# Optimization experiments

Measured on AMD Instinct MI355X. Metric: run time of the kernel, lower is better.

The kernel has to match this reference:

```python
import jax, jax.numpy as jnp
import numpy as np

B, H, W, DIM = 2, 64, 64, 128
NH = 4
HD = DIM // NH
KS = 7
DIL = 2
SCALE = HD ** -0.5


def _natten_idx(L, k, dil):
    """Per-position neighborhood start + rpb start (NATTEN semantics), as gather index tables."""
    ns = k // 2
    starts = np.empty(L, np.int32)
    pbs = np.empty(L, np.int32)
    for i in range(L):
        if dil <= 1:
            s = max(i - ns, 0) + (i + ns >= L) * (L - i - ns - 1)
            p = ns + (i < ns) * (ns - i) + (i + ns >= L) * (L - i - 1 - ns)
        else:
            if i - ns * dil < 0:
                s = i % dil
                p = k - 1 - (i // dil)
            elif i + ns * dil >= L:
                imodd = i % dil
                a = (L // dil) * dil
                b = L - a
                if imodd < b:
                    s = L - b + imodd - 2 * ns * dil
                else:
                    s = a + imodd - k * dil
                p = (L - i - 1) // dil
            else:
                s = i - ns * dil
                p = ns
        starts[i] = s
        pbs[i] = p
    key_idx = starts[:, None] + dil * np.arange(k, dtype=np.int32)  # [L, k] key positions
    pb_idx = pbs[:, None] + np.arange(k, dtype=np.int32)            # [L, k] rpb positions
    return key_idx, pb_idx


def setup_inputs() -> dict:
    key = jax.random.key(0)
    ks = jax.random.split(key, 12)
    shp = (B, H, W, DIM)
    q = jax.random.normal(ks[0], shp, jnp.float32)
    k = jax.random.normal(ks[1], shp, jnp.float32)
    v = jax.random.normal(ks[2], shp, jnp.float32)
    def lin(kk):
        return jax.random.normal(kk, (DIM, DIM), jnp.float32) * (DIM ** -0.5)
    Wq, Wk, Wv, Wo = lin(ks[3]), lin(ks[4]), lin(ks[5]), lin(ks[6])
    bq = jnp.zeros((DIM,), jnp.float32)
    bk = jnp.zeros((DIM,), jnp.float32)
    bv = jnp.zeros((DIM,), jnp.float32)
    bo = jnp.zeros((DIM,), jnp.float32)
    rpb = jax.random.normal(ks[7], (NH, 2 * KS - 1, 2 * KS - 1), jnp.float32) * 0.02
    return {"q": q, "k": k, "v": v, "Wq": Wq, "bq": bq, "Wk": Wk, "bk": bk,
            "Wv": Wv, "bv": bv, "rpb": rpb, "Wo": Wo, "bo": bo}


def _forward(q, k, v, Wq, bq, Wk, bk, Wv, bv, rpb, Wo, bo):
    Bc, Hc, Wc, C = q.shape
    ii, pi = _natten_idx(Hc, KS, DIL)   # [H, K]
    jj, pj = _natten_idx(Wc, KS, DIL)   # [W, K]

    def heads(x, Wm, bm):
        # [B,H,W,C] -> [B,NH,H,W,HD]
        return (x @ Wm + bm).reshape(Bc, Hc, Wc, NH, HD).transpose(0, 3, 1, 2, 4)

    qh = heads(q, Wq, bq) * SCALE
    kh = heads(k, Wk, bk)
    vh = heads(v, Wv, bv)

    # Gather KxK dilated neighborhoods: [B,NH,H,K,W,K,HD]
    knbr = kh[:, :, ii][:, :, :, :, jj]
    vnbr = vh[:, :, ii][:, :, :, :, jj]

    # attention logits per pixel over its KxK neighborhood: [B,NH,H,W,K,K]
    attn = jnp.einsum('bnhwd,bnhkwld->bnhwkl', qh, knbr)
    # relative position bias lookup: [NH,H,K,W,K] -> [NH,H,W,K,K]
    bias = rpb[:, pi][:, :, :, pj].transpose(0, 1, 3, 2, 4)
    attn = attn + bias[None]

    attn = jax.nn.softmax(attn.reshape(Bc, NH, Hc, Wc, KS * KS), axis=-1)
    attn = attn.reshape(Bc, NH, Hc, Wc, KS, KS)

    out = jnp.einsum('bnhwkl,bnhkwld->bnhwd', attn, vnbr)
    out = out.transpose(0, 2, 3, 1, 4).reshape(Bc, Hc, Wc, C)
    return out @ Wo + bo


def reference(q, k, v, Wq, bq, Wk, bk, Wv, bv, rpb, Wo, bo):
    return _forward(q, k, v, Wq, bq, Wk, bk, Wv, bv, rpb, Wo, bo)
```

## Files before the change

kernel.cpp:

```cpp
#include <hip/hip_runtime.h>
#include <hip/hip_bf16.h>
#include <math.h>

#define BB 2
#define HH 64
#define WW 64
#define DIMC 128
#define NH 4
#define HD 32
#define KS 7
#define DIL 2
#define NPIX (BB * HH * WW)
#define SCALE 0.17677669529663687f

typedef short bf16x8 __attribute__((ext_vector_type(8)));
typedef float f32x4  __attribute__((ext_vector_type(4)));

__device__ __forceinline__ short bf16r(float f) {
    union { float f; unsigned u; } x; x.f = f;
    unsigned r = x.u + 0x7FFF + ((x.u >> 16) & 1);
    return (short)(r >> 16);
}
__device__ __forceinline__ float uasf(unsigned u) {
    union { unsigned u; float f; } x; x.u = u; return x.f;
}

__global__ __launch_bounds__(256) void prep_w(
    const float* __restrict__ Wq, const float* __restrict__ Wk,
    const float* __restrict__ Wv, const float* __restrict__ Wo,
    short* __restrict__ Wt)
{
    const int z  = blockIdx.x >> 2;
    const int ks = blockIdx.x & 3;
    const float* W = (z == 0) ? Wq : (z == 1) ? Wk : (z == 2) ? Wv : Wo;

    __shared__ short T[32][136];
    const int t = threadIdx.x;
    const float4* Wg = (const float4*)(W + ks * 32 * 128);

    float4 xv[4];
#pragma unroll
    for (int u = 0; u < 4; ++u) xv[u] = Wg[u * 256 + t];
#pragma unroll
    for (int u = 0; u < 4; ++u) {
        const int e = u * 256 + t;
        const int r = e >> 5;
        const int c = (e & 31) * 4;
        short4 s4;
        s4.x = bf16r(xv[u].x); s4.y = bf16r(xv[u].y);
        s4.z = bf16r(xv[u].z); s4.w = bf16r(xv[u].w);
        *(short4*)&T[r][c] = s4;
    }
    __syncthreads();

    const int c = t >> 1;
    const int h = (t & 1) * 16;
    bf16x8 lo, hi;
#pragma unroll
    for (int i = 0; i < 8; ++i) { lo[i] = T[h + i][c]; hi[i] = T[h + 8 + i][c]; }
    short* outp = Wt + z * 16384 + c * 128 + ks * 32 + h;
    *(bf16x8*)(outp)     = lo;
    *(bf16x8*)(outp + 8) = hi;
}

__global__ __launch_bounds__(256) void qkv_mfma(
    const float* __restrict__ q, const float* __restrict__ k,
    const float* __restrict__ v, const short* __restrict__ Wt,
    const float* __restrict__ bq, const float* __restrict__ bk,
    const float* __restrict__ bv,
    float* __restrict__ qh, short* __restrict__ khb, short* __restrict__ vhb)
{
    const int z = blockIdx.y;
    const float* X    = (z == 0) ? q  : (z == 1) ? k  : v;
    const float* bias = (z == 0) ? bq : (z == 1) ? bk : bv;
    const short* Wz   = Wt + z * 16384;

    const int t    = threadIdx.x;
    const int wv   = t >> 6;
    const int lane = t & 63;
    const int lr   = lane & 15;
    const int lg   = lane >> 4;
    const int row0 = blockIdx.x * 32 + (wv & 1) * 16;
    const int col0 = (wv >> 1) * 64;

    bf16x8 bfr[16];
#pragma unroll
    for (int nt = 0; nt < 4; ++nt) {
        const short* wrow = Wz + (col0 + nt * 16 + lr) * 128 + lg * 8;
#pragma unroll
        for (int kk = 0; kk < 4; ++kk)
            bfr[nt * 4 + kk] = *(const bf16x8*)(wrow + kk * 32);
    }

    const float* xrow = X + (size_t)(row0 + lr) * 128 + lg * 8;
    bf16x8 a[4];
#pragma unroll
    for (int kk = 0; kk < 4; ++kk) {
        const float4 x0 = *(const float4*)(xrow + kk * 32);
        const float4 x1 = *(const float4*)(xrow + kk * 32 + 4);
        bf16x8 av;
        av[0] = bf16r(x0.x); av[1] = bf16r(x0.y);
        av[2] = bf16r(x0.z); av[3] = bf16r(x0.w);
        av[4] = bf16r(x1.x); av[5] = bf16r(x1.y);
        av[6] = bf16r(x1.z); av[7] = bf16r(x1.w);
        a[kk] = av;
    }

#pragma unroll
    for (int nt = 0; nt < 4; ++nt) {
        const int col = col0 + nt * 16 + lr;
        f32x4 acc = {0.f, 0.f, 0.f, 0.f};
#pragma unroll
        for (int kk = 0; kk < 4; ++kk)
            acc = __builtin_amdgcn_mfma_f32_16x16x32_bf16(a[kk], bfr[nt * 4 + kk], acc, 0, 0, 0);
        const float bc = bias[col];
        if (z == 0) {
#pragma unroll
            for (int jj = 0; jj < 4; ++jj)
                qh[(size_t)(row0 + lg * 4 + jj) * 128 + col] = (acc[jj] + bc) * SCALE;
        } else {
            short* Yb = (z == 1) ? khb : vhb;
#pragma unroll
            for (int jj = 0; jj < 4; ++jj)
                Yb[(size_t)(row0 + lg * 4 + jj) * 128 + col] = bf16r(acc[jj] + bc);
        }
    }
}

__device__ __forceinline__ void natten_idx(int i, int& s, int& p)
{
    if (i < 6) {
        s = i & 1;
        p = 6 - (i >> 1);
    } else if (i >= 58) {
        s = 50 + (i & 1);
        p = (63 - i) >> 1;
    } else {
        s = i - 6;
        p = 3;
    }
}

__global__ __launch_bounds__(256) void natten_out(
    const float* __restrict__ qh, const short* __restrict__ khb,
    const short* __restrict__ vhb, const float* __restrict__ rpb,
    const short* __restrict__ Wt, const float* __restrict__ bo,
    float* __restrict__ out)
{
    __shared__ short attS[16][136];

    const int blk  = blockIdx.x;
    const int work = (blk & 7) * 64 + (blk >> 3);
    const int t    = threadIdx.x;

    {
        const int lane4 = t & 3;
        const int n  = (t >> 2) & 3;
        const int p  = t >> 4;
        const int g  = work * 16 + p;
        const int j  = g & 63;
        const int i  = (g >> 6) & 63;
        const int b  = g >> 12;

        int si, pi0, sj, pj0;
        natten_idx(i, si, pi0);
        natten_idx(j, sj, pj0);

        const int coff = n * 32 + lane4 * 8;
        const size_t pixb = (size_t)(b * 4096 + i * 64 + j);
        const float4 q0 = *(const float4*)(qh + pixb * 128 + coff);
        const float4 q1 = *(const float4*)(qh + pixb * 128 + coff + 4);

        const float* rp = rpb + n * 169;

        float m = -1e30f, l = 0.0f;
        float o[8] = {0.f, 0.f, 0.f, 0.f, 0.f, 0.f, 0.f, 0.f};

#pragma unroll
        for (int ki = 0; ki < 7; ++ki) {
            const int iy = si + 2 * ki;
            const size_t rowbase = ((size_t)(b * 4096 + iy * 64)) * 128 + coff;
            const float* rrow = rp + (pi0 + ki) * 13 + pj0;

            float d[7];
#pragma unroll
            for (int kj = 0; kj < 7; ++kj) {
                const int ix = sj + 2 * kj;
                const uint4 kv = *(const uint4*)(khb + rowbase + (size_t)ix * 128);
                float dd =      q0.x * uasf(kv.x << 16);
                dd = fmaf(q0.y, uasf(kv.x & 0xFFFF0000u), dd);
                dd = fmaf(q0.z, uasf(kv.y << 16), dd);
                dd = fmaf(q0.w, uasf(kv.y & 0xFFFF0000u), dd);
                dd = fmaf(q1.x, uasf(kv.z << 16), dd);
                dd = fmaf(q1.y, uasf(kv.z & 0xFFFF0000u), dd);
                dd = fmaf(q1.z, uasf(kv.w << 16), dd);
                dd = fmaf(q1.w, uasf(kv.w & 0xFFFF0000u), dd);
                d[kj] = dd;
            }
#pragma unroll
            for (int kj = 0; kj < 7; ++kj) d[kj] += __shfl_xor(d[kj], 1);
#pragma unroll
            for (int kj = 0; kj < 7; ++kj) d[kj] += __shfl_xor(d[kj], 2);
#pragma unroll
            for (int kj = 0; kj < 7; ++kj) d[kj] += rrow[kj];

            const float g01 = fmaxf(d[0], d[1]);
            const float g23 = fmaxf(d[2], d[3]);
            const float g45 = fmaxf(d[4], d[5]);
            const float gm  = fmaxf(fmaxf(g01, g23), fmaxf(g45, d[6]));
            const float mn  = fmaxf(m, gm);
            const float corr = __expf(m - mn);
            m = mn;
            l *= corr;
#pragma unroll
            for (int e = 0; e < 8; ++e) o[e] *= corr;

#pragma unroll
            for (int kj = 0; kj < 7; ++kj) {
                const float pe = __expf(d[kj] - m);
                d[kj] = pe;
                l += pe;
            }

#pragma unroll
            for (int kj = 0; kj < 7; ++kj) {
                const int ix = sj + 2 * kj;
                const uint4 vv = *(const uint4*)(vhb + rowbase + (size_t)ix * 128);
                const float pe = d[kj];
                o[0] = fmaf(pe, uasf(vv.x << 16),          o[0]);
                o[1] = fmaf(pe, uasf(vv.x & 0xFFFF0000u),  o[1]);
                o[2] = fmaf(pe, uasf(vv.y << 16),          o[2]);
                o[3] = fmaf(pe, uasf(vv.y & 0xFFFF0000u),  o[3]);
                o[4] = fmaf(pe, uasf(vv.z << 16),          o[4]);
                o[5] = fmaf(pe, uasf(vv.z & 0xFFFF0000u),  o[5]);
                o[6] = fmaf(pe, uasf(vv.w << 16),          o[6]);
                o[7] = fmaf(pe, uasf(vv.w & 0xFFFF0000u),  o[7]);
            }
        }

        const float inv = 1.0f / l;
        bf16x8 ow;
#pragma unroll
        for (int e = 0; e < 8; ++e) ow[e] = bf16r(o[e] * inv);
        *(bf16x8*)&attS[p][coff] = ow;
    }

    __syncthreads();

    {
        const int wv   = t >> 6;
        const int lane = t & 63;
        const int lr   = lane & 15;
        const int lg   = lane >> 4;
        const int col0 = wv * 32;
        const short* Wz = Wt + 3 * 16384;

        bf16x8 bfr[8];
#pragma unroll
        for (int nt = 0; nt < 2; ++nt) {
            const short* wrow = Wz + (col0 + nt * 16 + lr) * 128 + lg * 8;
#pragma unroll
            for (int kk = 0; kk < 4; ++kk)
                bfr[nt * 4 + kk] = *(const bf16x8*)(wrow + kk * 32);
        }
        bf16x8 a[4];
#pragma unroll
        for (int kk = 0; kk < 4; ++kk)
            a[kk] = *(const bf16x8*)&attS[lr][kk * 32 + lg * 8];

#pragma unroll
        for (int nt = 0; nt < 2; ++nt) {
            const int col = col0 + nt * 16 + lr;
            f32x4 acc = {0.f, 0.f, 0.f, 0.f};
#pragma unroll
            for (int kk = 0; kk < 4; ++kk)
                acc = __builtin_amdgcn_mfma_f32_16x16x32_bf16(a[kk], bfr[nt * 4 + kk], acc, 0, 0, 0);
            const float bc = bo[col];
#pragma unroll
            for (int jj = 0; jj < 4; ++jj)
                out[(size_t)(work * 16 + lg * 4 + jj) * 128 + col] = acc[jj] + bc;
        }
    }
}

extern "C" void kernel_launch(void* const* d_in, const int* in_sizes, int n_in,
                              void* d_out, int out_size, void* d_ws, size_t ws_size,
                              hipStream_t stream)
{
    const float* q   = (const float*)d_in[0];
    const float* k   = (const float*)d_in[1];
    const float* v   = (const float*)d_in[2];
    const float* Wq  = (const float*)d_in[3];
    const float* bq  = (const float*)d_in[4];
    const float* Wk  = (const float*)d_in[5];
    const float* bk  = (const float*)d_in[6];
    const float* Wv  = (const float*)d_in[7];
    const float* bv  = (const float*)d_in[8];
    const float* rpb = (const float*)d_in[9];
    const float* Wo  = (const float*)d_in[10];
    const float* bo  = (const float*)d_in[11];

    float* ws   = (float*)d_ws;
    float* qh   = ws;
    short* khb  = (short*)(ws + (size_t)NPIX * 128);
    short* vhb  = khb + (size_t)NPIX * 128;
    short* Wt   = vhb + (size_t)NPIX * 128;
    float* out  = (float*)d_out;

    hipLaunchKernelGGL(prep_w, dim3(16), dim3(256), 0, stream, Wq, Wk, Wv, Wo, Wt);

    hipLaunchKernelGGL(qkv_mfma, dim3(256, 3), dim3(256), 0, stream,
                       q, k, v, Wt, bq, bk, bv, qh, khb, vhb);

    hipLaunchKernelGGL(natten_out, dim3(512), dim3(256), 0, stream,
                       qh, khb, vhb, rpb, Wt, bo, out);
}
```

Measured before the change: 35.20 us.

## Compute neighborhood attention with MFMA over a shared-memory key/value window

Replaces the per-pixel scalar FMA neighborhood attention with a block-level scheme: for each head, a 7x28 window of keys is staged into LDS, QK^T for 16 pixels is computed densely with bf16 MFMA, softmax is applied with masking into a sparse P matrix, and P·V is done with MFMA against a transposed V tile. The aim is to swap many redundant global loads and scalar FMAs for shared reuse and matrix instructions. In exchange it computes extra unused scores, rounds Q and P to bf16, adds several barriers per head and leaves many threads idle during softmax and PV.

```diff
diff --git a/kernel.cpp b/kernel.cpp
--- a/kernel.cpp
+++ b/kernel.cpp
@@ -21,9 +21,6 @@
     unsigned r = x.u + 0x7FFF + ((x.u >> 16) & 1);
     return (short)(r >> 16);
 }
-__device__ __forceinline__ float uasf(unsigned u) {
-    union { unsigned u; float f; } x; x.u = u; return x.f;
-}
 
 __global__ __launch_bounds__(256) void prep_w(
     const float* __restrict__ Wq, const float* __restrict__ Wk,
@@ -147,111 +144,159 @@
     const short* __restrict__ Wt, const float* __restrict__ bo,
     float* __restrict__ out)
 {
-    __shared__ short attS[16][136];
+    __shared__ __align__(16) short KT[208 * 40];
+    __shared__ __align__(16) float S[16 * 208];
+    __shared__ __align__(16) short P[16 * 232];
+    __shared__ __align__(16) short Vt[32 * 232];
+    __shared__ __align__(16) short attS[16][136];
 
     const int blk  = blockIdx.x;
     const int work = (blk & 7) * 64 + (blk >> 3);
     const int t    = threadIdx.x;
 
+    const int j0 = (work & 3) * 16;
+    const int i_ = (work >> 2) & 63;
+    const int b_ = work >> 8;
+
+    int si, pi0, sj0v, pj0v;
+    natten_idx(i_, si, pi0);
+    natten_idx(j0, sj0v, pj0v);
+    const int colbase = sj0v;
+
+    const int wv   = t >> 6;
+    const int lane = t & 63;
+    const int lr   = lane & 15;
+    const int lg   = lane >> 4;
+
+    const size_t gbase = (size_t)(b_ * 4096) * 128;
+
+#pragma unroll 1
+    for (int n = 0; n < 4; ++n) {
+        for (int u = t; u < 784; u += 256) {
+            const int key = u >> 2;
+            const int ch4 = (u & 3) * 8;
+            const int ki  = key / 28;
+            const int c   = key - ki * 28;
+            int col = colbase + c; col = (col > 63) ? 63 : col;
+            const int iy = si + 2 * ki;
+            const uint4 kv = *(const uint4*)(khb + gbase +
+                                 (size_t)(iy * 64 + col) * 128 + n * 32 + ch4);
+            *(uint4*)&KT[key * 40 + ch4] = kv;
+        }
+        __syncthreads();
+
+        {
+            const float* qp = qh + (size_t)(b_ * 4096 + i_ * 64 + j0 + lr) * 128
+                              + n * 32 + lg * 8;
+            const float4 x0 = *(const float4*)(qp);
+            const float4 x1 = *(const float4*)(qp + 4);
+            bf16x8 aq;
+            aq[0] = bf16r(x0.x); aq[1] = bf16r(x0.y);
+            aq[2] = bf16r(x0.z); aq[3] = bf16r(x0.w);
+            aq[4] = bf16r(x1.x); aq[5] = bf16r(x1.y);
+            aq[6] = bf16r(x1.z); aq[7] = bf16r(x1.w);
+
+            for (int nb = wv; nb < 13; nb += 4) {
+                const bf16x8 bk = *(const bf16x8*)&KT[(nb * 16 + lr) * 40 + lg * 8];
+                f32x4 sa = {0.f, 0.f, 0.f, 0.f};
+                sa = __builtin_amdgcn_mfma_f32_16x16x32_bf16(aq, bk, sa, 0, 0, 0);
+#pragma unroll
+                for (int jj = 0; jj < 4; ++jj)
+                    S[(lg * 4 + jj) * 208 + nb * 16 + lr] = sa[jj];
+            }
+            unsigned* Pz = (unsigned*)P;
+            for (int u = t; u < 1856; u += 256) Pz[u] = 0u;
+        }
+        __syncthreads();
+
+        if (t < 64) {
+            const int px = t >> 2, q = t & 3;
+            const int j = j0 + px;
+            int sjp, pj0p;
+            natten_idx(j, sjp, pj0p);
+            const int cj0 = sjp - colbase;
+
+            float d[14];
+            float mx = -1e30f;
+#pragma unroll
+            for (int rr = 0; rr < 2; ++rr) {
+                const int ki  = q + rr * 4;
+                const bool ok = (ki < 7);
+                const int kis = ok ? ki : 3;
+                const float* rp = rpb + n * 169 + (pi0 + kis) * 13 + pj0p;
+#pragma unroll
+                for (int kj = 0; kj < 7; ++kj) {
+                    const float s = ok ? (S[px * 208 + kis * 28 + cj0 + 2 * kj] + rp[kj])
+                                       : -1e30f;
+                    d[rr * 7 + kj] = s;
+                    mx = fmaxf(mx, s);
+                }
+            }
+            mx = fmaxf(mx, __shfl_xor(mx, 1));
+            mx = fmaxf(mx, __shfl_xor(mx, 2));
+            float l = 0.f;
+#pragma unroll
+            for (int ii = 0; ii < 14; ++ii) {
+                const float pe = __expf(d[ii] - mx);
+                d[ii] = pe;
+                l += pe;
+            }
+            l += __shfl_xor(l, 1);
+            l += __shfl_xor(l, 2);
+            const float inv = 1.0f / l;
+#pragma unroll
+            for (int rr = 0; rr < 2; ++rr) {
+                const int ki  = q + rr * 4;
+                if (ki < 7) {
+#pragma unroll
+                    for (int kj = 0; kj < 7; ++kj)
+                        P[px * 232 + ki * 28 + cj0 + 2 * kj] = bf16r(d[rr * 7 + kj] * inv);
+                }
+            }
+        } else {
+            for (int u = t - 64; u < 896; u += 192) {
+                const int key = u >> 2;
+                const int ch4 = (u & 3) * 8;
+                if (key < 196) {
+                    const int ki = key / 28;
+                    const int c  = key - ki * 28;
+                    int col = colbase + c; col = (col > 63) ? 63 : col;
+                    const int iy = si + 2 * ki;
+                    const uint4 vv = *(const uint4*)(vhb + gbase +
+                                       (size_t)(iy * 64 + col) * 128 + n * 32 + ch4);
+                    Vt[(ch4 + 0) * 232 + key] = (short)(vv.x & 0xFFFFu);
+                    Vt[(ch4 + 1) * 232 + key] = (short)(vv.x >> 16);
+                    Vt[(ch4 + 2) * 232 + key] = (short)(vv.y & 0xFFFFu);
+                    Vt[(ch4 + 3) * 232 + key] = (short)(vv.y >> 16);
+                    Vt[(ch4 + 4) * 232 + key] = (short)(vv.z & 0xFFFFu);
+                    Vt[(ch4 + 5) * 232 + key] = (short)(vv.z >> 16);
+                    Vt[(ch4 + 6) * 232 + key] = (short)(vv.w & 0xFFFFu);
+                    Vt[(ch4 + 7) * 232 + key] = (short)(vv.w >> 16);
+                } else {
+#pragma unroll
+                    for (int e = 0; e < 8; ++e)
+                        Vt[(ch4 + e) * 232 + key] = 0;
+                }
+            }
+        }
+        __syncthreads();
+
+        if (wv < 2) {
+            f32x4 oa = {0.f, 0.f, 0.f, 0.f};
+#pragma unroll
+            for (int kk = 0; kk < 7; ++kk) {
+                const bf16x8 pa = *(const bf16x8*)&P[lr * 232 + kk * 32 + lg * 8];
+                const bf16x8 vb = *(const bf16x8*)&Vt[(wv * 16 + lr) * 232 + kk * 32 + lg * 8];
+                oa = __builtin_amdgcn_mfma_f32_16x16x32_bf16(pa, vb, oa, 0, 0, 0);
+            }
+#pragma unroll
+            for (int jj = 0; jj < 4; ++jj)
+                attS[lg * 4 + jj][n * 32 + wv * 16 + lr] = bf16r(oa[jj]);
+        }
+        __syncthreads();
+    }
+
     {
-        const int lane4 = t & 3;
-        const int n  = (t >> 2) & 3;
-        const int p  = t >> 4;
-        const int g  = work * 16 + p;
-        const int j  = g & 63;
-        const int i  = (g >> 6) & 63;
-        const int b  = g >> 12;
-
-        int si, pi0, sj, pj0;
-        natten_idx(i, si, pi0);
-        natten_idx(j, sj, pj0);
-
-        const int coff = n * 32 + lane4 * 8;
-        const size_t pixb = (size_t)(b * 4096 + i * 64 + j);
-        const float4 q0 = *(const float4*)(qh + pixb * 128 + coff);
-        const float4 q1 = *(const float4*)(qh + pixb * 128 + coff + 4);
-
-        const float* rp = rpb + n * 169;
-
-        float m = -1e30f, l = 0.0f;
-        float o[8] = {0.f, 0.f, 0.f, 0.f, 0.f, 0.f, 0.f, 0.f};
-
-#pragma unroll
-        for (int ki = 0; ki < 7; ++ki) {
-            const int iy = si + 2 * ki;
-            const size_t rowbase = ((size_t)(b * 4096 + iy * 64)) * 128 + coff;
-            const float* rrow = rp + (pi0 + ki) * 13 + pj0;
-
-            float d[7];
-#pragma unroll
-            for (int kj = 0; kj < 7; ++kj) {
-                const int ix = sj + 2 * kj;
-                const uint4 kv = *(const uint4*)(khb + rowbase + (size_t)ix * 128);
-                float dd =      q0.x * uasf(kv.x << 16);
-                dd = fmaf(q0.y, uasf(kv.x & 0xFFFF0000u), dd);
-                dd = fmaf(q0.z, uasf(kv.y << 16), dd);
-                dd = fmaf(q0.w, uasf(kv.y & 0xFFFF0000u), dd);
-                dd = fmaf(q1.x, uasf(kv.z << 16), dd);
-                dd = fmaf(q1.y, uasf(kv.z & 0xFFFF0000u), dd);
-                dd = fmaf(q1.z, uasf(kv.w << 16), dd);
-                dd = fmaf(q1.w, uasf(kv.w & 0xFFFF0000u), dd);
-                d[kj] = dd;
-            }
-#pragma unroll
-            for (int kj = 0; kj < 7; ++kj) d[kj] += __shfl_xor(d[kj], 1);
-#pragma unroll
-            for (int kj = 0; kj < 7; ++kj) d[kj] += __shfl_xor(d[kj], 2);
-#pragma unroll
-            for (int kj = 0; kj < 7; ++kj) d[kj] += rrow[kj];
-
-            const float g01 = fmaxf(d[0], d[1]);
-            const float g23 = fmaxf(d[2], d[3]);
-            const float g45 = fmaxf(d[4], d[5]);
-            const float gm  = fmaxf(fmaxf(g01, g23), fmaxf(g45, d[6]));
-            const float mn  = fmaxf(m, gm);
-            const float corr = __expf(m - mn);
-            m = mn;
-            l *= corr;
-#pragma unroll
-            for (int e = 0; e < 8; ++e) o[e] *= corr;
-
-#pragma unroll
-            for (int kj = 0; kj < 7; ++kj) {
-                const float pe = __expf(d[kj] - m);
-                d[kj] = pe;
-                l += pe;
-            }
-
-#pragma unroll
-            for (int kj = 0; kj < 7; ++kj) {
-                const int ix = sj + 2 * kj;
-                const uint4 vv = *(const uint4*)(vhb + rowbase + (size_t)ix * 128);
-                const float pe = d[kj];
-                o[0] = fmaf(pe, uasf(vv.x << 16),          o[0]);
-                o[1] = fmaf(pe, uasf(vv.x & 0xFFFF0000u),  o[1]);
-                o[2] = fmaf(pe, uasf(vv.y << 16),          o[2]);
-                o[3] = fmaf(pe, uasf(vv.y & 0xFFFF0000u),  o[3]);
-                o[4] = fmaf(pe, uasf(vv.z << 16),          o[4]);
-                o[5] = fmaf(pe, uasf(vv.z & 0xFFFF0000u),  o[5]);
-                o[6] = fmaf(pe, uasf(vv.w << 16),          o[6]);
-                o[7] = fmaf(pe, uasf(vv.w & 0xFFFF0000u),  o[7]);
-            }
-        }
-
-        const float inv = 1.0f / l;
-        bf16x8 ow;
-#pragma unroll
-        for (int e = 0; e < 8; ++e) ow[e] = bf16r(o[e] * inv);
-        *(bf16x8*)&attS[p][coff] = ow;
-    }
-
-    __syncthreads();
-
-    {
-        const int wv   = t >> 6;
-        const int lane = t & 63;
-        const int lr   = lane & 15;
-        const int lg   = lane >> 4;
         const int col0 = wv * 32;
         const short* Wz = Wt + 3 * 16384;
 
```

Result: slower. 43.40 us (+23.3%).
